# Optimization experiments

Hardware: AMD Instinct MI355X
Metric: run time of the kernel (lower is better)

The kernel has to match this reference:

```python
import jax, jax.numpy as jnp
import numpy as np

B, N, D = 8, 512, 512          # batch, seq_len, n_units (== d_in for residual)
H = 8                          # n_heads
DH = D // H                    # head dim
POS_CLIP = 60
EPS = 1e-7


def setup_inputs() -> dict:
    key = jax.random.key(0)
    ks = jax.random.split(key, 16)
    s = 0.02
    inp = {
        "query": jax.random.normal(ks[0], (B, N, D), dtype=jnp.float32),
        "valid_len": jax.random.randint(ks[1], (B,), 256, N + 1, dtype=jnp.int32),
        "Wq": jax.random.normal(ks[2], (D, D), dtype=jnp.float32) * s,
        "bq": jnp.zeros((D,), jnp.float32),
        "Wk": jax.random.normal(ks[3], (D, D), dtype=jnp.float32) * s,
        "bk": jnp.zeros((D,), jnp.float32),
        "Wv": jax.random.normal(ks[4], (D, D), dtype=jnp.float32) * s,
        "bv": jnp.zeros((D,), jnp.float32),
        "Wh": jax.random.normal(ks[5], (D, D), dtype=jnp.float32) * s,
        "bh": jnp.zeros((D,), jnp.float32),
        "pos_k": jax.random.uniform(ks[6], (2 * POS_CLIP + 1, DH), dtype=jnp.float32, minval=-0.05, maxval=0.05),
        "conv1_w": jax.random.normal(ks[7], (5, 5, H, 2 * H), dtype=jnp.float32) * s,  # HWIO
        "conv1_b": jnp.zeros((2 * H,), jnp.float32),
        "norm1_gamma": jnp.ones((2 * H,), jnp.float32),
        "norm1_beta": jnp.zeros((2 * H,), jnp.float32),
        "conv2_w": jax.random.normal(ks[8], (5, 5, 2 * H, H), dtype=jnp.float32) * s,
        "conv2_b": jnp.zeros((H,), jnp.float32),
        "ln_gamma": jnp.ones((D,), jnp.float32),
        "ln_beta": jnp.zeros((D,), jnp.float32),
    }
    return inp


def _conv_same(x, k, b):
    # x: [b, n, n, cin], k: [kh, kw, cin, cout] -> [b, n, n, cout]
    y = jax.lax.conv_general_dilated(x, k, window_strides=(1, 1), padding="SAME",
                                     dimension_numbers=("NHWC", "HWIO", "NHWC"))
    return y + b


def _norm_masked(x, valid_len, gamma, beta):
    # Norm(axes=[1,2]) with tf.nn.weighted_moments; mask over the query axis (axis 1).
    b, n, m, c = x.shape
    w = (jnp.arange(n)[None, :] < valid_len[:, None]).astype(x.dtype)  # [b, n]
    w4 = w[:, :, None, None]
    sw = valid_len.astype(x.dtype)[:, None, None, None] * m            # sum of broadcast weights
    mean = jnp.sum(w4 * x, axis=(1, 2), keepdims=True) / sw
    var = jnp.sum(w4 * (x - mean) ** 2, axis=(1, 2), keepdims=True) / sw
    return gamma * (x - mean) * jax.lax.rsqrt(var + EPS) + beta


def reference(query, valid_len, Wq, bq, Wk, bk, Wv, bv, Wh, bh, pos_k,
              conv1_w, conv1_b, norm1_gamma, norm1_beta, conv2_w, conv2_b,
              ln_gamma, ln_beta):
    b, n, d_in = query.shape
    # relative position indices (Shaw et al.), clipped to +/- POS_CLIP
    rel = jnp.clip(jnp.arange(n)[None, :] - jnp.arange(n)[:, None], -POS_CLIP, POS_CLIP) + POS_CLIP
    pos_enc = pos_k[rel]                                   # [n, n, dh]

    def heads(x):
        # tf.concat(tf.split(x, H, -1), 0): head-major blocks of size b
        return x.reshape(b, n, H, DH).transpose(2, 0, 1, 3)  # [h, b, n, dh]

    q = heads(query @ Wq + bq)
    k = heads(query @ Wk + bk)
    v = heads(query @ Wv + bv)

    scores = jnp.einsum("hbnd,hbmd->hbnm", q, k) + jnp.einsum("hbnd,nmd->hbnm", q, pos_enc)
    scores = scores / jnp.sqrt(jnp.asarray(DH, scores.dtype))

    # SelfCNN over attention maps: [b, n, n, h]
    maps = scores.transpose(1, 2, 3, 0)
    y = _conv_same(maps, conv1_w, conv1_b)
    y = _norm_masked(y, valid_len, norm1_gamma, norm1_beta)
    y = jax.nn.relu(y)
    y = _conv_same(y, conv2_w, conv2_b)                    # [b, n, n, h]
    scores = y.transpose(3, 0, 1, 2)                       # [h, b, n, m]

    seq_mask = jnp.arange(n)[None, :] < valid_len[:, None]  # [b, n] over key axis
    scores = jnp.where(seq_mask[None, :, None, :], scores, jnp.asarray(-1e12, scores.dtype))
    attn = jax.nn.softmax(scores, axis=-1)

    out = jnp.einsum("hbnm,hbmd->hbnd", attn, v)
    out = out.transpose(1, 2, 0, 3).reshape(b, n, H * DH)  # merge heads back
    out = out @ Wh + bh + query                            # residual

    mean = jnp.mean(out, axis=-1, keepdims=True)
    var = jnp.var(out, axis=-1, keepdims=True)
    return ln_gamma * (out - mean) * jax.lax.rsqrt(var + EPS) + ln_beta
```

## Files before the change

kernel.cpp:

```cpp
#include <hip/hip_runtime.h>

#define PC_ 60

typedef unsigned short u16;
typedef __attribute__((ext_vector_type(8))) short short8v;
typedef __attribute__((ext_vector_type(4))) float f32x4;

__device__ inline float bf2f(u16 u) {
    union { unsigned int i; float f; } x; x.i = ((unsigned)u) << 16; return x.f;
}
__device__ inline u16 f2bf(float f) {
    union { float f; unsigned int i; } x; x.f = f;
    unsigned int r = x.i + 0x7fff + ((x.i >> 16) & 1);
    return (u16)(r >> 16);
}
__device__ inline unsigned pk2(float a, float b) {
    return (unsigned)f2bf(a) | ((unsigned)f2bf(b) << 16);
}

__global__ __launch_bounds__(256) void k_prepx(const float* __restrict__ X, u16* __restrict__ Xb)
{
    const int i = (blockIdx.x * 256 + threadIdx.x) * 8;
    float4 a = *reinterpret_cast<const float4*>(X + i);
    float4 b = *reinterpret_cast<const float4*>(X + i + 4);
    *reinterpret_cast<uint4*>(Xb + i) =
        make_uint4(pk2(a.x, a.y), pk2(a.z, a.w), pk2(b.x, b.y), pk2(b.z, b.w));
}

__global__ __launch_bounds__(256) void k_prept(
    const float* __restrict__ W0, const float* __restrict__ W1,
    const float* __restrict__ W2, const float* __restrict__ W3,
    u16* __restrict__ T0, u16* __restrict__ T1, u16* __restrict__ T2, u16* __restrict__ T3)
{
    const int z = blockIdx.z;
    const float* W = (z == 0) ? W0 : (z == 1) ? W1 : (z == 2) ? W2 : W3;
    u16* T        = (z == 0) ? T0 : (z == 1) ? T1 : (z == 2) ? T2 : T3;
    __shared__ float ls[64 * 65];
    const int k0 = blockIdx.x * 64, n0 = blockIdx.y * 64;
    const int t = threadIdx.x;
#pragma unroll
    for (int i = 0; i < 16; ++i) {
        const int idx = t + i * 256, r = idx >> 6, c = idx & 63;
        ls[c * 65 + r] = W[(size_t)(k0 + r) * 512 + n0 + c];
    }
    __syncthreads();
#pragma unroll
    for (int i = 0; i < 16; ++i) {
        const int idx = t + i * 256, r = idx >> 6, c = idx & 63;
        T[(size_t)(n0 + r) * 512 + k0 + c] = f2bf(ls[r * 65 + c]);
    }
}

__global__ void k_wprep(const float* __restrict__ c1w, const float* __restrict__ c2w,
                        const float* __restrict__ pos_k,
                        u16* __restrict__ Wf1, u16* __restrict__ Wf2, u16* __restrict__ pos_kb)
{
    const int t = threadIdx.x;
    for (int s = t; s < 448; s += 256) {
        const int q = s >> 6, l = s & 63, lg = l >> 4, n = l & 15;
        const int G = q * 4 + lg;
        unsigned o[4];
#pragma unroll
        for (int u2 = 0; u2 < 4; ++u2) {
            float v0 = 0.f, v1 = 0.f;
            if (G < 25) {
                const int dn = G / 5, dm = G - dn * 5;
                v0 = c1w[((dn * 5 + dm) * 8 + u2 * 2 + 0) * 16 + n];
                v1 = c1w[((dn * 5 + dm) * 8 + u2 * 2 + 1) * 16 + n];
            }
            o[u2] = pk2(v0, v1);
        }
        *reinterpret_cast<uint4*>(&Wf1[s * 8]) = make_uint4(o[0], o[1], o[2], o[3]);
    }
    for (int s = t; s < 832; s += 256) {
        const int q = s >> 6, l = s & 63, lg = l >> 4, n = l & 15;
        const int G = q * 4 + lg;
        unsigned o[4];
#pragma unroll
        for (int u2 = 0; u2 < 4; ++u2) {
            float v0 = 0.f, v1 = 0.f;
            if (G < 50 && n < 8) {
                const int pos = G >> 1, h = G & 1;
                const int dn = pos / 5, dm = pos - dn * 5;
                v0 = c2w[((dn * 5 + dm) * 16 + h * 8 + u2 * 2 + 0) * 8 + n];
                v1 = c2w[((dn * 5 + dm) * 16 + h * 8 + u2 * 2 + 1) * 8 + n];
            }
            o[u2] = pk2(v0, v1);
        }
        *reinterpret_cast<uint4*>(&Wf2[s * 8]) = make_uint4(o[0], o[1], o[2], o[3]);
    }
    for (int s = t; s < 128 * 64; s += 256) {
        const int r = s >> 6;
        pos_kb[s] = (r < 121) ? f2bf(pos_k[s]) : (u16)0;
    }
}

__global__ __launch_bounds__(256) void k_qkvm(
    const u16* __restrict__ Xb,
    const u16* __restrict__ WT0, const u16* __restrict__ WT1, const u16* __restrict__ WT2,
    const float* __restrict__ b0, const float* __restrict__ b1, const float* __restrict__ b2,
    u16* __restrict__ Qb, u16* __restrict__ Kb, u16* __restrict__ Vt)
{
    const int z = blockIdx.z;
    const u16* WT    = (z == 0) ? WT0 : (z == 1) ? WT1 : WT2;
    const float* bias = (z == 0) ? b0 : (z == 1) ? b1 : b2;
    __shared__ __align__(16) u16 sh[18432];
    u16* As = sh; u16* Bs = sh + 9216;
    const int t = threadIdx.x, lane = t & 63, wave = t >> 6;
    const int wm = wave >> 1, wn = wave & 1;
    const int lg = lane >> 4, ln16 = lane & 15;
    const int m0 = blockIdx.x * 128, n0 = blockIdx.y * 128;
    f32x4 acc[4][4] = {};
    for (int k0 = 0; k0 < 512; k0 += 64) {
#pragma unroll
        for (int u = 0; u < 4; ++u) {
            const int chunk = u * 256 + t, row = chunk >> 3, ko = (chunk & 7) * 8;
            *reinterpret_cast<uint4*>(As + row * 72 + ko) =
                *reinterpret_cast<const uint4*>(Xb + (size_t)(m0 + row) * 512 + k0 + ko);
            *reinterpret_cast<uint4*>(Bs + row * 72 + ko) =
                *reinterpret_cast<const uint4*>(WT + (size_t)(n0 + row) * 512 + k0 + ko);
        }
        __syncthreads();
#pragma unroll
        for (int kk = 0; kk < 64; kk += 32) {
            short8v a[4], bfr[4];
#pragma unroll
            for (int mi = 0; mi < 4; ++mi)
                a[mi] = *reinterpret_cast<const short8v*>(As + (wm * 64 + mi * 16 + ln16) * 72 + kk + lg * 8);
#pragma unroll
            for (int ni = 0; ni < 4; ++ni)
                bfr[ni] = *reinterpret_cast<const short8v*>(Bs + (wn * 64 + ni * 16 + ln16) * 72 + kk + lg * 8);
#pragma unroll
            for (int mi = 0; mi < 4; ++mi)
#pragma unroll
                for (int ni = 0; ni < 4; ++ni)
                    acc[mi][ni] = __builtin_amdgcn_mfma_f32_16x16x32_bf16(a[mi], bfr[ni], acc[mi][ni], 0, 0, 0);
        }
        __syncthreads();
    }
    u16* Cs = sh + wave * 4608;
#pragma unroll
    for (int ni = 0; ni < 4; ++ni) {
        const float bv = bias[n0 + wn * 64 + ni * 16 + ln16];
#pragma unroll
        for (int mi = 0; mi < 4; ++mi)
#pragma unroll
            for (int r = 0; r < 4; ++r)
                Cs[(mi * 16 + lg * 4 + r) * 72 + ni * 16 + ln16] = f2bf(acc[mi][ni][r] + bv);
    }
    if (z < 2) {
        u16* O = (z == 0) ? Qb : Kb;
#pragma unroll
        for (int j = 0; j < 8; ++j) {
            const int chunk = j * 64 + lane, row = chunk >> 3, co = (chunk & 7) * 8;
            const int tok = m0 + wm * 64 + row;
            const int b = tok >> 9, n = tok & 511;
            const int cg = n0 + wn * 64 + co;
            const int h = cg >> 6, dh = cg & 63;
            *reinterpret_cast<uint4*>(O + ((size_t)((b * 8 + h) * 512 + n)) * 64 + dh) =
                *reinterpret_cast<const uint4*>(Cs + row * 72 + co);
        }
    } else {
#pragma unroll
        for (int j = 0; j < 8; ++j) {
            const int chunk = j * 64 + lane, dr = chunk >> 3, no8 = (chunk & 7) * 8;
            const int cg = n0 + wn * 64 + dr;
            const int h = cg >> 6, dh = cg & 63;
            const int tok = m0 + wm * 64 + no8;
            const int b = tok >> 9, n = tok & 511;
            u16 v[8];
#pragma unroll
            for (int e = 0; e < 8; ++e) v[e] = Cs[(no8 + e) * 72 + dr];
            uint4 o = make_uint4((unsigned)v[0] | ((unsigned)v[1] << 16),
                                 (unsigned)v[2] | ((unsigned)v[3] << 16),
                                 (unsigned)v[4] | ((unsigned)v[5] << 16),
                                 (unsigned)v[6] | ((unsigned)v[7] << 16));
            *reinterpret_cast<uint4*>(Vt + ((size_t)((b * 8 + h) * 64 + dh)) * 512 + n) = o;
        }
    }
}

__global__ __launch_bounds__(256) void k_qposm(
    const u16* __restrict__ Qb, const u16* __restrict__ pos_kb, u16* __restrict__ QP)
{
    __shared__ __align__(16) u16 sh[18432];
    u16* As = sh; u16* Bs = sh + 9216;
    const int t = threadIdx.x, lane = t & 63, wave = t >> 6;
    const int lg = lane >> 4, ln16 = lane & 15;
    const int n0 = blockIdx.x * 128, bh = blockIdx.y;
#pragma unroll
    for (int u = 0; u < 4; ++u) {
        const int chunk = u * 256 + t, row = chunk >> 3, ko = (chunk & 7) * 8;
        *reinterpret_cast<uint4*>(As + row * 72 + ko) =
            *reinterpret_cast<const uint4*>(Qb + ((size_t)(bh * 512 + n0 + row)) * 64 + ko);
        *reinterpret_cast<uint4*>(Bs + row * 72 + ko) =
            *reinterpret_cast<const uint4*>(pos_kb + (size_t)row * 64 + ko);
    }
    __syncthreads();
    f32x4 acc[2][8] = {};
#pragma unroll
    for (int kk = 0; kk < 64; kk += 32) {
        short8v a[2], bfr[8];
#pragma unroll
        for (int mi = 0; mi < 2; ++mi)
            a[mi] = *reinterpret_cast<const short8v*>(As + (wave * 32 + mi * 16 + ln16) * 72 + kk + lg * 8);
#pragma unroll
        for (int ni = 0; ni < 8; ++ni)
            bfr[ni] = *reinterpret_cast<const short8v*>(Bs + (ni * 16 + ln16) * 72 + kk + lg * 8);
#pragma unroll
        for (int mi = 0; mi < 2; ++mi)
#pragma unroll
            for (int ni = 0; ni < 8; ++ni)
                acc[mi][ni] = __builtin_amdgcn_mfma_f32_16x16x32_bf16(a[mi], bfr[ni], acc[mi][ni], 0, 0, 0);
    }
    __syncthreads();
    u16* Cs = sh + wave * 4352;
#pragma unroll
    for (int mi = 0; mi < 2; ++mi)
#pragma unroll
        for (int ni = 0; ni < 8; ++ni)
#pragma unroll
            for (int r = 0; r < 4; ++r)
                Cs[(mi * 16 + lg * 4 + r) * 136 + ni * 16 + ln16] = f2bf(acc[mi][ni][r]);
#pragma unroll
    for (int j = 0; j < 8; ++j) {
        const int chunk = j * 64 + lane, row = chunk >> 4, co = (chunk & 15) * 8;
        *reinterpret_cast<uint4*>(QP + ((size_t)(bh * 512 + n0 + wave * 32 + row)) * 128 + co) =
            *reinterpret_cast<const uint4*>(Cs + row * 136 + co);
    }
}

__global__ __launch_bounds__(256) void k_scoresm(
    const u16* __restrict__ Qb, const u16* __restrict__ Kb, const u16* __restrict__ QP,
    u16* __restrict__ S)
{
    __shared__ __align__(16) u16 sh[18432];
    u16* As = sh; u16* Bs = sh + 9216;
    const int t = threadIdx.x, lane = t & 63, wave = t >> 6;
    const int wm = wave >> 1, wn = wave & 1;
    const int lg = lane >> 4, ln16 = lane & 15;
    const int m0 = blockIdx.x * 128, n0 = blockIdx.y * 128, bh = blockIdx.z;
#pragma unroll
    for (int u = 0; u < 4; ++u) {
        const int chunk = u * 256 + t, row = chunk >> 3, ko = (chunk & 7) * 8;
        *reinterpret_cast<uint4*>(As + row * 72 + ko) =
            *reinterpret_cast<const uint4*>(Qb + ((size_t)(bh * 512 + n0 + row)) * 64 + ko);
        *reinterpret_cast<uint4*>(Bs + row * 72 + ko) =
            *reinterpret_cast<const uint4*>(Kb + ((size_t)(bh * 512 + m0 + row)) * 64 + ko);
    }
    __syncthreads();
    f32x4 acc[4][4] = {};
#pragma unroll
    for (int kk = 0; kk < 64; kk += 32) {
        short8v a[4], bfr[4];
#pragma unroll
        for (int mi = 0; mi < 4; ++mi)
            a[mi] = *reinterpret_cast<const short8v*>(As + (wm * 64 + mi * 16 + ln16) * 72 + kk + lg * 8);
#pragma unroll
        for (int ni = 0; ni < 4; ++ni)
            bfr[ni] = *reinterpret_cast<const short8v*>(Bs + (wn * 64 + ni * 16 + ln16) * 72 + kk + lg * 8);
#pragma unroll
        for (int mi = 0; mi < 4; ++mi)
#pragma unroll
            for (int ni = 0; ni < 4; ++ni)
                acc[mi][ni] = __builtin_amdgcn_mfma_f32_16x16x32_bf16(a[mi], bfr[ni], acc[mi][ni], 0, 0, 0);
    }
    __syncthreads();
    u16* QPs = sh;
#pragma unroll
    for (int u = 0; u < 8; ++u) {
        const int chunk = u * 256 + t, row = chunk >> 4, co = (chunk & 15) * 8;
        *reinterpret_cast<uint4*>(QPs + row * 128 + co) =
            *reinterpret_cast<const uint4*>(QP + ((size_t)(bh * 512 + n0 + row)) * 128 + co);
    }
    __syncthreads();
#pragma unroll
    for (int mi = 0; mi < 4; ++mi)
#pragma unroll
        for (int ni = 0; ni < 4; ++ni) {
            const int m_g = m0 + wn * 64 + ni * 16 + ln16;
#pragma unroll
            for (int r = 0; r < 4; ++r) {
                const int n_loc = wm * 64 + mi * 16 + lg * 4 + r;
                const int n_g = n0 + n_loc;
                int rel = m_g - n_g;
                rel = rel < -PC_ ? -PC_ : (rel > PC_ ? PC_ : rel);
                const float v = (acc[mi][ni][r] + bf2f(QPs[n_loc * 128 + rel + PC_])) * 0.125f;
                S[(size_t)bh * 262144 + (size_t)n_g * 512 + m_g] = f2bf(v);
            }
        }
}

__global__ __launch_bounds__(256) void k_conv1m(
    const u16* __restrict__ S, const u16* __restrict__ Wf,
    const float* __restrict__ bias, u16* __restrict__ Y,
    const int* __restrict__ VL, float* __restrict__ ST)
{
    __shared__ __align__(16) u16 xs[10368];
    __shared__ float wred[4][16][2];
    const int t = threadIdx.x;
    const int b = blockIdx.z;
    const int n0 = blockIdx.y * 32;
    const int m0 = blockIdx.x * 32;
    const u16* sp0 = S + (size_t)(b * 8) * 262144;
    for (int idx = t; idx < 1296; idx += 256) {
        const int r = idx / 36; const int c = idx - r * 36;
        const int gn = n0 - 2 + r, gm = m0 - 2 + c;
        uint4 pk = make_uint4(0, 0, 0, 0);
        if ((unsigned)gn < 512u && (unsigned)gm < 512u) {
            const u16* p = sp0 + (size_t)gn * 512 + gm;
            u16 v[8];
#pragma unroll
            for (int e = 0; e < 8; ++e) v[e] = p[(size_t)e * 262144];
            pk.x = (unsigned)v[0] | ((unsigned)v[1] << 16);
            pk.y = (unsigned)v[2] | ((unsigned)v[3] << 16);
            pk.z = (unsigned)v[4] | ((unsigned)v[5] << 16);
            pk.w = (unsigned)v[6] | ((unsigned)v[7] << 16);
        }
        *reinterpret_cast<uint4*>(&xs[idx * 8]) = pk;
    }
    const int lane = t & 63, wave = t >> 6;
    const int lg = lane >> 4, ln16 = lane & 15;
    short8v bq[7];
#pragma unroll
    for (int q = 0; q < 7; ++q)
        bq[q] = *reinterpret_cast<const short8v*>(&Wf[(q * 64 + lane) * 8]);
    int aoff[7];
#pragma unroll
    for (int q = 0; q < 7; ++q) {
        const int G = q * 4 + lg; const int p = (G < 25) ? G : 0;
        const int dn = p / 5, dm = p - dn * 5;
        aoff[q] = (dn * 36 + dm) * 8;
    }
    const float bs = bias[ln16];
    const int vl = VL[b];
    float sst = 0.f, sst2 = 0.f;
    __syncthreads();
    for (int i = 0; i < 16; ++i) {
        const int j = wave * 16 + i;
        const int tr = j >> 1, c0 = (j & 1) << 4;
        const int pb = (tr * 36 + c0 + ln16) * 8;
        f32x4 acc = {bs, bs, bs, bs};
#pragma unroll
        for (int q = 0; q < 7; ++q) {
            short8v a = *reinterpret_cast<const short8v*>(&xs[pb + aoff[q]]);
            acc = __builtin_amdgcn_mfma_f32_16x16x32_bf16(a, bq[q], acc, 0, 0, 0);
        }
        u16* yp = Y + (((size_t)(b * 512 + n0 + tr)) * 512 + (m0 + c0 + lg * 4)) * 16 + ln16;
        yp[0]  = f2bf(acc[0]); yp[16] = f2bf(acc[1]);
        yp[32] = f2bf(acc[2]); yp[48] = f2bf(acc[3]);
        if (n0 + tr < vl) {
            sst  += acc[0] + acc[1] + acc[2] + acc[3];
            sst2 += acc[0]*acc[0] + acc[1]*acc[1] + acc[2]*acc[2] + acc[3]*acc[3];
        }
    }
    sst  += __shfl_xor(sst, 16);  sst  += __shfl_xor(sst, 32);
    sst2 += __shfl_xor(sst2, 16); sst2 += __shfl_xor(sst2, 32);
    if (lane < 16) { wred[wave][lane][0] = sst; wred[wave][lane][1] = sst2; }
    __syncthreads();
    if (t < 16) {
        const float a  = wred[0][t][0] + wred[1][t][0] + wred[2][t][0] + wred[3][t][0];
        const float b2 = wred[0][t][1] + wred[1][t][1] + wred[2][t][1] + wred[3][t][1];
        atomicAdd(&ST[(b * 16 + t) * 2 + 0], a);
        atomicAdd(&ST[(b * 16 + t) * 2 + 1], b2);
    }
}

__global__ void k_statfin(const float* __restrict__ ST, const int* __restrict__ VL,
                          const float* __restrict__ g, const float* __restrict__ be,
                          float* __restrict__ ST2)
{
    const int i = threadIdx.x;
    if (i < 128) {
        const int b = i >> 4, c = i & 15;
        const float sw = (float)VL[b] * 512.f;
        const float mean = ST[i * 2] / sw;
        const float var = ST[i * 2 + 1] / sw - mean * mean;
        const float scale = g[c] * rsqrtf(var + 1e-7f);
        ST2[i * 2] = scale;
        ST2[i * 2 + 1] = be[c] - mean * scale;
    }
}

__global__ __launch_bounds__(256) void k_conv2m(
    const u16* __restrict__ Y, const float* __restrict__ ST2,
    const u16* __restrict__ Wf, const float* __restrict__ bias,
    u16* __restrict__ S2)
{
    __shared__ __align__(16) u16 xs[20736];
    const int t = threadIdx.x;
    const int b = blockIdx.z;
    const int n0 = blockIdx.y * 32, m0 = blockIdx.x * 32;
    float sc[16], shv[16];
#pragma unroll
    for (int ch = 0; ch < 16; ++ch) {
        sc[ch]  = ST2[(b * 16 + ch) * 2 + 0];
        shv[ch] = ST2[(b * 16 + ch) * 2 + 1];
    }
    for (int idx = t; idx < 1296; idx += 256) {
        const int r = idx / 36; const int c = idx - r * 36;
        const int gn = n0 - 2 + r, gm = m0 - 2 + c;
        uint4 p0 = make_uint4(0, 0, 0, 0), p1 = p0;
        if ((unsigned)gn < 512u && (unsigned)gm < 512u) {
            const u16* yp = Y + (((size_t)(b * 512 + gn)) * 512 + gm) * 16;
            const uint4 r0 = *reinterpret_cast<const uint4*>(yp);
            const uint4 r1 = *reinterpret_cast<const uint4*>(yp + 8);
            const unsigned w0[4] = {r0.x, r0.y, r0.z, r0.w};
            const unsigned w1[4] = {r1.x, r1.y, r1.z, r1.w};
            unsigned o0[4], o1[4];
#pragma unroll
            for (int u2 = 0; u2 < 4; ++u2) {
                const int ch = u2 * 2;
                float a0 = bf2f((u16)(w0[u2] & 0xffff));
                float a1 = bf2f((u16)(w0[u2] >> 16));
                a0 = fmaf(a0, sc[ch], shv[ch]);          a0 = a0 > 0.f ? a0 : 0.f;
                a1 = fmaf(a1, sc[ch + 1], shv[ch + 1]);  a1 = a1 > 0.f ? a1 : 0.f;
                o0[u2] = pk2(a0, a1);
                const int ch2 = 8 + u2 * 2;
                float b0 = bf2f((u16)(w1[u2] & 0xffff));
                float b1 = bf2f((u16)(w1[u2] >> 16));
                b0 = fmaf(b0, sc[ch2], shv[ch2]);          b0 = b0 > 0.f ? b0 : 0.f;
                b1 = fmaf(b1, sc[ch2 + 1], shv[ch2 + 1]);  b1 = b1 > 0.f ? b1 : 0.f;
                o1[u2] = pk2(b0, b1);
            }
            p0 = make_uint4(o0[0], o0[1], o0[2], o0[3]);
            p1 = make_uint4(o1[0], o1[1], o1[2], o1[3]);
        }
        *reinterpret_cast<uint4*>(&xs[idx * 8]) = p0;
        *reinterpret_cast<uint4*>(&xs[10368 + idx * 8]) = p1;
    }
    const int lane = t & 63, wave = t >> 6;
    const int lg = lane >> 4, ln16 = lane & 15;
    short8v bq[13];
#pragma unroll
    for (int q = 0; q < 13; ++q)
        bq[q] = *reinterpret_cast<const short8v*>(&Wf[(q * 64 + lane) * 8]);
    int aoff[13];
#pragma unroll
    for (int q = 0; q < 13; ++q) {
        const int G = q * 4 + lg; const int p = (G < 50) ? G : 0;
        const int pos = p >> 1, h = p & 1;
        const int dn = pos / 5, dm = pos - dn * 5;
        aoff[q] = h * 10368 + (dn * 36 + dm) * 8;
    }
    const float bs = (ln16 < 8) ? bias[ln16] : 0.f;
    __syncthreads();
    for (int i = 0; i < 16; ++i) {
        const int j = wave * 16 + i;
        const int tr = j >> 1, c0 = (j & 1) << 4;
        const int pb = (tr * 36 + c0 + ln16) * 8;
        f32x4 acc = {bs, bs, bs, bs};
#pragma unroll
        for (int q = 0; q < 13; ++q) {
            short8v a = *reinterpret_cast<const short8v*>(&xs[pb + aoff[q]]);
            acc = __builtin_amdgcn_mfma_f32_16x16x32_bf16(a, bq[q], acc, 0, 0, 0);
        }
        if (ln16 < 8) {
            uint2 o = make_uint2(pk2(acc[0], acc[1]), pk2(acc[2], acc[3]));
            *reinterpret_cast<uint2*>(
                &S2[(((size_t)(b * 8 + ln16)) * 512 + n0 + tr) * 512 + m0 + c0 + lg * 4]) = o;
        }
    }
}

__global__ __launch_bounds__(256) void k_softmax(u16* __restrict__ S,
                                                 const int* __restrict__ VL)
{
    const int row = blockIdx.x * 4 + (threadIdx.x >> 6);
    const int lane = threadIdx.x & 63;
    const int b = row >> 12;
    const int vl = VL[b];
    u16* p = S + (size_t)row * 512;
    uint4 v = *reinterpret_cast<const uint4*>(p + lane * 8);
    const unsigned w[4] = {v.x, v.y, v.z, v.w};
    float vals[8];
#pragma unroll
    for (int j = 0; j < 4; ++j) {
        vals[2 * j]     = bf2f((u16)(w[j] & 0xffff));
        vals[2 * j + 1] = bf2f((u16)(w[j] >> 16));
    }
    const int mbase = lane * 8;
    float mx = -3.0e38f;
#pragma unroll
    for (int j = 0; j < 8; ++j) {
        if (mbase + j >= vl) vals[j] = -3.0e38f;
        mx = fmaxf(mx, vals[j]);
    }
#pragma unroll
    for (int o = 32; o; o >>= 1) mx = fmaxf(mx, __shfl_xor(mx, o));
    float sum = 0.f;
#pragma unroll
    for (int j = 0; j < 8; ++j) {
        const float e = __expf(vals[j] - mx);
        vals[j] = e;
        sum += e;
    }
#pragma unroll
    for (int o = 32; o; o >>= 1) sum += __shfl_xor(sum, o);
    const float inv = 1.0f / sum;
    uint4 ov = make_uint4(pk2(vals[0] * inv, vals[1] * inv), pk2(vals[2] * inv, vals[3] * inv),
                          pk2(vals[4] * inv, vals[5] * inv), pk2(vals[6] * inv, vals[7] * inv));
    *reinterpret_cast<uint4*>(p + lane * 8) = ov;
}

__global__ __launch_bounds__(256) void k_avm(
    const u16* __restrict__ P, const u16* __restrict__ Vt, u16* __restrict__ X2)
{
    __shared__ __align__(16) u16 sh[13824];
    u16* As = sh; u16* Bs = sh + 9216;
    const int t = threadIdx.x, lane = t & 63, wave = t >> 6;
    const int lg = lane >> 4, ln16 = lane & 15;
    const int n0 = blockIdx.x * 128, bh = blockIdx.y;
    const int b = bh >> 3, h = bh & 7;
    f32x4 acc[2][4] = {};
    for (int k0 = 0; k0 < 512; k0 += 64) {
#pragma unroll
        for (int u = 0; u < 4; ++u) {
            const int chunk = u * 256 + t, row = chunk >> 3, ko = (chunk & 7) * 8;
            *reinterpret_cast<uint4*>(As + row * 72 + ko) =
                *reinterpret_cast<const uint4*>(P + ((size_t)(bh * 512 + n0 + row)) * 512 + k0 + ko);
        }
#pragma unroll
        for (int u = 0; u < 2; ++u) {
            const int chunk = u * 256 + t, row = chunk >> 3, ko = (chunk & 7) * 8;
            *reinterpret_cast<uint4*>(Bs + row * 72 + ko) =
                *reinterpret_cast<const uint4*>(Vt + ((size_t)(bh * 64 + row)) * 512 + k0 + ko);
        }
        __syncthreads();
#pragma unroll
        for (int kk = 0; kk < 64; kk += 32) {
            short8v a[2], bfr[4];
#pragma unroll
            for (int mi = 0; mi < 2; ++mi)
                a[mi] = *reinterpret_cast<const short8v*>(As + (wave * 32 + mi * 16 + ln16) * 72 + kk + lg * 8);
#pragma unroll
            for (int ni = 0; ni < 4; ++ni)
                bfr[ni] = *reinterpret_cast<const short8v*>(Bs + (ni * 16 + ln16) * 72 + kk + lg * 8);
#pragma unroll
            for (int mi = 0; mi < 2; ++mi)
#pragma unroll
                for (int ni = 0; ni < 4; ++ni)
                    acc[mi][ni] = __builtin_amdgcn_mfma_f32_16x16x32_bf16(a[mi], bfr[ni], acc[mi][ni], 0, 0, 0);
        }
        __syncthreads();
    }
    u16* Cs = sh + wave * 2304;
#pragma unroll
    for (int mi = 0; mi < 2; ++mi)
#pragma unroll
        for (int ni = 0; ni < 4; ++ni)
#pragma unroll
            for (int r = 0; r < 4; ++r)
                Cs[(mi * 16 + lg * 4 + r) * 72 + ni * 16 + ln16] = f2bf(acc[mi][ni][r]);
#pragma unroll
    for (int j = 0; j < 4; ++j) {
        const int chunk = j * 64 + lane, row = chunk >> 3, co = (chunk & 7) * 8;
        const int tn = n0 + wave * 32 + row;
        *reinterpret_cast<uint4*>(X2 + ((size_t)(b * 512 + tn)) * 512 + h * 64 + co) =
            *reinterpret_cast<const uint4*>(Cs + row * 72 + co);
    }
}

__global__ __launch_bounds__(256) void k_outm(
    const u16* __restrict__ X2, const u16* __restrict__ WT, const float* __restrict__ bias,
    const float* __restrict__ Xq, float* __restrict__ Pout)
{
    __shared__ __align__(16) u16 sh[18432];
    u16* As = sh; u16* Bs = sh + 9216;
    const int t = threadIdx.x, lane = t & 63, wave = t >> 6;
    const int wm = wave >> 1, wn = wave & 1;
    const int lg = lane >> 4, ln16 = lane & 15;
    const int m0 = blockIdx.x * 128, n0 = blockIdx.y * 128;
    f32x4 acc[4][4] = {};
    for (int k0 = 0; k0 < 512; k0 += 64) {
#pragma unroll
        for (int u = 0; u < 4; ++u) {
            const int chunk = u * 256 + t, row = chunk >> 3, ko = (chunk & 7) * 8;
            *reinterpret_cast<uint4*>(As + row * 72 + ko) =
                *reinterpret_cast<const uint4*>(X2 + (size_t)(m0 + row) * 512 + k0 + ko);
            *reinterpret_cast<uint4*>(Bs + row * 72 + ko) =
                *reinterpret_cast<const uint4*>(WT + (size_t)(n0 + row) * 512 + k0 + ko);
        }
        __syncthreads();
#pragma unroll
        for (int kk = 0; kk < 64; kk += 32) {
            short8v a[4], bfr[4];
#pragma unroll
            for (int mi = 0; mi < 4; ++mi)
                a[mi] = *reinterpret_cast<const short8v*>(As + (wm * 64 + mi * 16 + ln16) * 72 + kk + lg * 8);
#pragma unroll
            for (int ni = 0; ni < 4; ++ni)
                bfr[ni] = *reinterpret_cast<const short8v*>(Bs + (wn * 64 + ni * 16 + ln16) * 72 + kk + lg * 8);
#pragma unroll
            for (int mi = 0; mi < 4; ++mi)
#pragma unroll
                for (int ni = 0; ni < 4; ++ni)
                    acc[mi][ni] = __builtin_amdgcn_mfma_f32_16x16x32_bf16(a[mi], bfr[ni], acc[mi][ni], 0, 0, 0);
        }
        __syncthreads();
    }
#pragma unroll
    for (int ni = 0; ni < 4; ++ni) {
        const int cg = n0 + wn * 64 + ni * 16 + ln16;
        const float bv = bias[cg];
#pragma unroll
        for (int mi = 0; mi < 4; ++mi)
#pragma unroll
            for (int r = 0; r < 4; ++r) {
                const int tok = m0 + wm * 64 + mi * 16 + lg * 4 + r;
                Pout[(size_t)tok * 512 + cg] = acc[mi][ni][r] + bv + Xq[(size_t)tok * 512 + cg];
            }
    }
}

__global__ __launch_bounds__(256) void k_ln(
    const float* __restrict__ P, const float* __restrict__ g,
    const float* __restrict__ be, float* __restrict__ out)
{
    const int row = blockIdx.x * 4 + (threadIdx.x >> 6);
    const int lane = threadIdx.x & 63;
    const float* p = P + (size_t)row * 512;
    float4 v0 = reinterpret_cast<const float4*>(p)[lane];
    float4 v1 = reinterpret_cast<const float4*>(p)[64 + lane];
    float s = v0.x + v0.y + v0.z + v0.w + v1.x + v1.y + v1.z + v1.w;
#pragma unroll
    for (int o = 32; o; o >>= 1) s += __shfl_xor(s, o);
    const float mean = s * (1.0f / 512.0f);
    float d[8] = {v0.x - mean, v0.y - mean, v0.z - mean, v0.w - mean,
                  v1.x - mean, v1.y - mean, v1.z - mean, v1.w - mean};
    float s2 = 0.f;
#pragma unroll
    for (int j = 0; j < 8; ++j) s2 += d[j] * d[j];
#pragma unroll
    for (int o = 32; o; o >>= 1) s2 += __shfl_xor(s2, o);
    const float rstd = rsqrtf(s2 * (1.0f / 512.0f) + 1e-7f);
    float4 g0 = reinterpret_cast<const float4*>(g)[lane];
    float4 g1 = reinterpret_cast<const float4*>(g)[64 + lane];
    float4 b0 = reinterpret_cast<const float4*>(be)[lane];
    float4 b1 = reinterpret_cast<const float4*>(be)[64 + lane];
    float* op = out + (size_t)row * 512;
    reinterpret_cast<float4*>(op)[lane] =
        make_float4(d[0] * rstd * g0.x + b0.x, d[1] * rstd * g0.y + b0.y,
                    d[2] * rstd * g0.z + b0.z, d[3] * rstd * g0.w + b0.w);
    reinterpret_cast<float4*>(op)[64 + lane] =
        make_float4(d[4] * rstd * g1.x + b1.x, d[5] * rstd * g1.y + b1.y,
                    d[6] * rstd * g1.z + b1.z, d[7] * rstd * g1.w + b1.w);
}

extern "C" void kernel_launch(void* const* d_in, const int* in_sizes, int n_in,
                              void* d_out, int out_size, void* d_ws, size_t ws_size,
                              hipStream_t stream)
{
    const float* query = (const float*)d_in[0];
    const int*   VL    = (const int*)d_in[1];
    const float* Wq = (const float*)d_in[2];  const float* bq = (const float*)d_in[3];
    const float* Wk = (const float*)d_in[4];  const float* bk = (const float*)d_in[5];
    const float* Wv = (const float*)d_in[6];  const float* bv = (const float*)d_in[7];
    const float* Wh = (const float*)d_in[8];  const float* bh = (const float*)d_in[9];
    const float* pos_k = (const float*)d_in[10];
    const float* c1w = (const float*)d_in[11]; const float* c1b = (const float*)d_in[12];
    const float* n1g = (const float*)d_in[13]; const float* n1b = (const float*)d_in[14];
    const float* c2w = (const float*)d_in[15]; const float* c2b = (const float*)d_in[16];
    const float* lng = (const float*)d_in[17]; const float* lnb = (const float*)d_in[18];

    float* ws = (float*)d_ws;
    const size_t M1 = (size_t)1 << 20;
    u16* S1  = (u16*)ws;
    u16* Y1  = (u16*)(ws + 8 * M1);
    u16* Xb  = (u16*)(ws + 24 * M1);
    u16* Qb  = (u16*)(ws + 25 * M1);
    u16* Kb  = (u16*)(ws + 26 * M1);
    u16* Vt  = (u16*)(ws + 27 * M1);
    u16* QPb = (u16*)(ws + 28 * M1);
    u16* WqT = (u16*)(ws + 30 * M1);
    u16* WkT = WqT + 262144;
    u16* WvT = WkT + 262144;
    u16* WhT = WvT + 262144;
    u16* pos_kb = (u16*)(ws + 30 * M1 + 524288);
    u16* Wf1 = pos_kb + 8192;
    u16* Wf2 = Wf1 + 3584;
    float* ST  = ws + 31 * M1;
    float* ST2 = ST + 256;
    u16* X2 = Xb;
    float* Pout = ws + 28 * M1;

    hipMemsetAsync(ST, 0, 256 * sizeof(float), stream);

    k_prepx<<<1024, 256, 0, stream>>>(query, Xb);
    k_prept<<<dim3(8, 8, 4), 256, 0, stream>>>(Wq, Wk, Wv, Wh, WqT, WkT, WvT, WhT);
    k_wprep<<<1, 256, 0, stream>>>(c1w, c2w, pos_k, Wf1, Wf2, pos_kb);
    k_qkvm<<<dim3(32, 4, 3), 256, 0, stream>>>(Xb, WqT, WkT, WvT, bq, bk, bv, Qb, Kb, Vt);
    k_qposm<<<dim3(4, 64), 256, 0, stream>>>(Qb, pos_kb, QPb);
    k_scoresm<<<dim3(4, 4, 64), 256, 0, stream>>>(Qb, Kb, QPb, S1);
    k_conv1m<<<dim3(16, 16, 8), 256, 0, stream>>>(S1, Wf1, c1b, Y1, VL, ST);
    k_statfin<<<1, 128, 0, stream>>>(ST, VL, n1g, n1b, ST2);
    k_conv2m<<<dim3(16, 16, 8), 256, 0, stream>>>(Y1, ST2, Wf2, c2b, S1);
    k_softmax<<<8192, 256, 0, stream>>>(S1, VL);
    k_avm<<<dim3(4, 64), 256, 0, stream>>>(S1, Vt, X2);
    k_outm<<<dim3(32, 4), 256, 0, stream>>>(X2, WhT, bh, query, Pout);
    k_ln<<<1024, 256, 0, stream>>>(Pout, lng, lnb, (float*)d_out);
}
```

Measured before the change: 286.5 us.

## Fuse conv1 recompute into conv2, fuse softmax into AV, merge weight prep

Conv1 now runs twice. The first pass only gathers normalization statistics, writes no Y1, and skips tiles past valid_len. The second pass recomputes conv1 on a halo tile inside the conv2 kernel, so the 16-channel intermediate never goes to or from global memory. Softmax is folded into the AV GEMM: row max and sum are computed first and the probabilities are rebuilt on the fly while loading the A tiles. The weight-prep kernel is merged into the transpose kernel as an extra z-slice. This trades extra conv1 MFMA work, 67KB of dynamic shared memory (which limits occupancy) and a second exp pass for much less memory traffic and fewer launches.

```diff
diff --git a/kernel.cpp b/kernel.cpp
--- a/kernel.cpp
+++ b/kernel.cpp
@@ -30,14 +30,58 @@
 __global__ __launch_bounds__(256) void k_prept(
     const float* __restrict__ W0, const float* __restrict__ W1,
     const float* __restrict__ W2, const float* __restrict__ W3,
-    u16* __restrict__ T0, u16* __restrict__ T1, u16* __restrict__ T2, u16* __restrict__ T3)
+    u16* __restrict__ T0, u16* __restrict__ T1, u16* __restrict__ T2, u16* __restrict__ T3,
+    const float* __restrict__ c1w, const float* __restrict__ c2w,
+    const float* __restrict__ pos_k,
+    u16* __restrict__ Wf1, u16* __restrict__ Wf2, u16* __restrict__ pos_kb)
 {
     const int z = blockIdx.z;
+    const int t = threadIdx.x;
+    if (z == 4) {
+        if (blockIdx.x != 0 || blockIdx.y != 0) return;
+        for (int s = t; s < 448; s += 256) {
+            const int q = s >> 6, l = s & 63, lg = l >> 4, n = l & 15;
+            const int G = q * 4 + lg;
+            unsigned o[4];
+#pragma unroll
+            for (int u2 = 0; u2 < 4; ++u2) {
+                float v0 = 0.f, v1 = 0.f;
+                if (G < 25) {
+                    const int dn = G / 5, dm = G - dn * 5;
+                    v0 = c1w[((dn * 5 + dm) * 8 + u2 * 2 + 0) * 16 + n];
+                    v1 = c1w[((dn * 5 + dm) * 8 + u2 * 2 + 1) * 16 + n];
+                }
+                o[u2] = pk2(v0, v1);
+            }
+            *reinterpret_cast<uint4*>(&Wf1[s * 8]) = make_uint4(o[0], o[1], o[2], o[3]);
+        }
+        for (int s = t; s < 832; s += 256) {
+            const int q = s >> 6, l = s & 63, lg = l >> 4, n = l & 15;
+            const int G = q * 4 + lg;
+            unsigned o[4];
+#pragma unroll
+            for (int u2 = 0; u2 < 4; ++u2) {
+                float v0 = 0.f, v1 = 0.f;
+                if (G < 50 && n < 8) {
+                    const int pos = G >> 1, h = G & 1;
+                    const int dn = pos / 5, dm = pos - dn * 5;
+                    v0 = c2w[((dn * 5 + dm) * 16 + h * 8 + u2 * 2 + 0) * 8 + n];
+                    v1 = c2w[((dn * 5 + dm) * 16 + h * 8 + u2 * 2 + 1) * 8 + n];
+                }
+                o[u2] = pk2(v0, v1);
+            }
+            *reinterpret_cast<uint4*>(&Wf2[s * 8]) = make_uint4(o[0], o[1], o[2], o[3]);
+        }
+        for (int s = t; s < 128 * 64; s += 256) {
+            const int r = s >> 6;
+            pos_kb[s] = (r < 121) ? f2bf(pos_k[s]) : (u16)0;
+        }
+        return;
+    }
     const float* W = (z == 0) ? W0 : (z == 1) ? W1 : (z == 2) ? W2 : W3;
     u16* T        = (z == 0) ? T0 : (z == 1) ? T1 : (z == 2) ? T2 : T3;
     __shared__ float ls[64 * 65];
     const int k0 = blockIdx.x * 64, n0 = blockIdx.y * 64;
-    const int t = threadIdx.x;
 #pragma unroll
     for (int i = 0; i < 16; ++i) {
         const int idx = t + i * 256, r = idx >> 6, c = idx & 63;
@@ -48,50 +92,6 @@
     for (int i = 0; i < 16; ++i) {
         const int idx = t + i * 256, r = idx >> 6, c = idx & 63;
         T[(size_t)(n0 + r) * 512 + k0 + c] = f2bf(ls[r * 65 + c]);
-    }
-}
-
-__global__ void k_wprep(const float* __restrict__ c1w, const float* __restrict__ c2w,
-                        const float* __restrict__ pos_k,
-                        u16* __restrict__ Wf1, u16* __restrict__ Wf2, u16* __restrict__ pos_kb)
-{
-    const int t = threadIdx.x;
-    for (int s = t; s < 448; s += 256) {
-        const int q = s >> 6, l = s & 63, lg = l >> 4, n = l & 15;
-        const int G = q * 4 + lg;
-        unsigned o[4];
-#pragma unroll
-        for (int u2 = 0; u2 < 4; ++u2) {
-            float v0 = 0.f, v1 = 0.f;
-            if (G < 25) {
-                const int dn = G / 5, dm = G - dn * 5;
-                v0 = c1w[((dn * 5 + dm) * 8 + u2 * 2 + 0) * 16 + n];
-                v1 = c1w[((dn * 5 + dm) * 8 + u2 * 2 + 1) * 16 + n];
-            }
-            o[u2] = pk2(v0, v1);
-        }
-        *reinterpret_cast<uint4*>(&Wf1[s * 8]) = make_uint4(o[0], o[1], o[2], o[3]);
-    }
-    for (int s = t; s < 832; s += 256) {
-        const int q = s >> 6, l = s & 63, lg = l >> 4, n = l & 15;
-        const int G = q * 4 + lg;
-        unsigned o[4];
-#pragma unroll
-        for (int u2 = 0; u2 < 4; ++u2) {
-            float v0 = 0.f, v1 = 0.f;
-            if (G < 50 && n < 8) {
-                const int pos = G >> 1, h = G & 1;
-                const int dn = pos / 5, dm = pos - dn * 5;
-                v0 = c2w[((dn * 5 + dm) * 16 + h * 8 + u2 * 2 + 0) * 8 + n];
-                v1 = c2w[((dn * 5 + dm) * 16 + h * 8 + u2 * 2 + 1) * 8 + n];
-            }
-            o[u2] = pk2(v0, v1);
-        }
-        *reinterpret_cast<uint4*>(&Wf2[s * 8]) = make_uint4(o[0], o[1], o[2], o[3]);
-    }
-    for (int s = t; s < 128 * 64; s += 256) {
-        const int r = s >> 6;
-        pos_kb[s] = (r < 121) ? f2bf(pos_k[s]) : (u16)0;
     }
 }
 
@@ -291,10 +291,10 @@
         }
 }
 
-__global__ __launch_bounds__(256) void k_conv1m(
+__global__ __launch_bounds__(256) void k_stats1(
     const u16* __restrict__ S, const u16* __restrict__ Wf,
-    const float* __restrict__ bias, u16* __restrict__ Y,
-    const int* __restrict__ VL, float* __restrict__ ST)
+    const float* __restrict__ bias, const int* __restrict__ VL,
+    float* __restrict__ ST)
 {
     __shared__ __align__(16) u16 xs[10368];
     __shared__ float wred[4][16][2];
@@ -302,6 +302,8 @@
     const int b = blockIdx.z;
     const int n0 = blockIdx.y * 32;
     const int m0 = blockIdx.x * 32;
+    const int vl = VL[b];
+    if (n0 >= vl) return;
     const u16* sp0 = S + (size_t)(b * 8) * 262144;
     for (int idx = t; idx < 1296; idx += 256) {
         const int r = idx / 36; const int c = idx - r * 36;
@@ -333,7 +335,6 @@
         aoff[q] = (dn * 36 + dm) * 8;
     }
     const float bs = bias[ln16];
-    const int vl = VL[b];
     float sst = 0.f, sst2 = 0.f;
     __syncthreads();
     for (int i = 0; i < 16; ++i) {
@@ -346,9 +347,6 @@
             short8v a = *reinterpret_cast<const short8v*>(&xs[pb + aoff[q]]);
             acc = __builtin_amdgcn_mfma_f32_16x16x32_bf16(a, bq[q], acc, 0, 0, 0);
         }
-        u16* yp = Y + (((size_t)(b * 512 + n0 + tr)) * 512 + (m0 + c0 + lg * 4)) * 16 + ln16;
-        yp[0]  = f2bf(acc[0]); yp[16] = f2bf(acc[1]);
-        yp[32] = f2bf(acc[2]); yp[48] = f2bf(acc[3]);
         if (n0 + tr < vl) {
             sst  += acc[0] + acc[1] + acc[2] + acc[3];
             sst2 += acc[0]*acc[0] + acc[1]*acc[1] + acc[2]*acc[2] + acc[3]*acc[3];
@@ -382,78 +380,102 @@
     }
 }
 
-__global__ __launch_bounds__(256) void k_conv2m(
-    const u16* __restrict__ Y, const float* __restrict__ ST2,
-    const u16* __restrict__ Wf, const float* __restrict__ bias,
+__global__ __launch_bounds__(256) void k_fused12(
+    const u16* __restrict__ S, const float* __restrict__ ST2,
+    const u16* __restrict__ Wf1, const float* __restrict__ c1b,
+    const u16* __restrict__ Wf2, const float* __restrict__ c2b,
     u16* __restrict__ S2)
 {
-    __shared__ __align__(16) u16 xs[20736];
+    extern __shared__ __align__(16) u16 dsm[];
+    u16* xs = dsm;
+    u16* ys = dsm + 12800;
     const int t = threadIdx.x;
     const int b = blockIdx.z;
     const int n0 = blockIdx.y * 32, m0 = blockIdx.x * 32;
-    float sc[16], shv[16];
-#pragma unroll
-    for (int ch = 0; ch < 16; ++ch) {
-        sc[ch]  = ST2[(b * 16 + ch) * 2 + 0];
-        shv[ch] = ST2[(b * 16 + ch) * 2 + 1];
-    }
-    for (int idx = t; idx < 1296; idx += 256) {
-        const int r = idx / 36; const int c = idx - r * 36;
-        const int gn = n0 - 2 + r, gm = m0 - 2 + c;
-        uint4 p0 = make_uint4(0, 0, 0, 0), p1 = p0;
+    const u16* sp0 = S + (size_t)(b * 8) * 262144;
+    for (int idx = t; idx < 1600; idx += 256) {
+        const int r = idx / 40; const int c = idx - r * 40;
+        const int gn = n0 - 4 + r, gm = m0 - 4 + c;
+        uint4 pk = make_uint4(0, 0, 0, 0);
         if ((unsigned)gn < 512u && (unsigned)gm < 512u) {
-            const u16* yp = Y + (((size_t)(b * 512 + gn)) * 512 + gm) * 16;
-            const uint4 r0 = *reinterpret_cast<const uint4*>(yp);
-            const uint4 r1 = *reinterpret_cast<const uint4*>(yp + 8);
-            const unsigned w0[4] = {r0.x, r0.y, r0.z, r0.w};
-            const unsigned w1[4] = {r1.x, r1.y, r1.z, r1.w};
-            unsigned o0[4], o1[4];
-#pragma unroll
-            for (int u2 = 0; u2 < 4; ++u2) {
-                const int ch = u2 * 2;
-                float a0 = bf2f((u16)(w0[u2] & 0xffff));
-                float a1 = bf2f((u16)(w0[u2] >> 16));
-                a0 = fmaf(a0, sc[ch], shv[ch]);          a0 = a0 > 0.f ? a0 : 0.f;
-                a1 = fmaf(a1, sc[ch + 1], shv[ch + 1]);  a1 = a1 > 0.f ? a1 : 0.f;
-                o0[u2] = pk2(a0, a1);
-                const int ch2 = 8 + u2 * 2;
-                float b0 = bf2f((u16)(w1[u2] & 0xffff));
-                float b1 = bf2f((u16)(w1[u2] >> 16));
-                b0 = fmaf(b0, sc[ch2], shv[ch2]);          b0 = b0 > 0.f ? b0 : 0.f;
-                b1 = fmaf(b1, sc[ch2 + 1], shv[ch2 + 1]);  b1 = b1 > 0.f ? b1 : 0.f;
-                o1[u2] = pk2(b0, b1);
-            }
-            p0 = make_uint4(o0[0], o0[1], o0[2], o0[3]);
-            p1 = make_uint4(o1[0], o1[1], o1[2], o1[3]);
-        }
-        *reinterpret_cast<uint4*>(&xs[idx * 8]) = p0;
-        *reinterpret_cast<uint4*>(&xs[10368 + idx * 8]) = p1;
+            const u16* p = sp0 + (size_t)gn * 512 + gm;
+            u16 v[8];
+#pragma unroll
+            for (int e = 0; e < 8; ++e) v[e] = p[(size_t)e * 262144];
+            pk.x = (unsigned)v[0] | ((unsigned)v[1] << 16);
+            pk.y = (unsigned)v[2] | ((unsigned)v[3] << 16);
+            pk.z = (unsigned)v[4] | ((unsigned)v[5] << 16);
+            pk.w = (unsigned)v[6] | ((unsigned)v[7] << 16);
+        }
+        *reinterpret_cast<uint4*>(&xs[idx * 8]) = pk;
     }
     const int lane = t & 63, wave = t >> 6;
     const int lg = lane >> 4, ln16 = lane & 15;
-    short8v bq[13];
+    short8v bq1[7];
+#pragma unroll
+    for (int q = 0; q < 7; ++q)
+        bq1[q] = *reinterpret_cast<const short8v*>(&Wf1[(q * 64 + lane) * 8]);
+    int aoff1[7];
+#pragma unroll
+    for (int q = 0; q < 7; ++q) {
+        const int G = q * 4 + lg; const int p = (G < 25) ? G : 0;
+        const int dn = p / 5, dm = p - dn * 5;
+        aoff1[q] = (dn * 40 + dm) * 8;
+    }
+    const float bs1 = c1b[ln16];
+    const float scn = ST2[(b * 16 + ln16) * 2 + 0];
+    const float shn = ST2[(b * 16 + ln16) * 2 + 1];
+    const int yhalf = (ln16 >> 3) * 10368;
+    const int ych = ln16 & 7;
+    __syncthreads();
+    for (int i = 0; i < 21; ++i) {
+        const int j = i * 4 + wave;
+        if (j >= 81) break;
+        const int pa = j * 16 + ln16;
+        const int arow = pa / 36, acol = pa - arow * 36;
+        const int abase = (arow * 40 + acol) * 8;
+        f32x4 acc = {bs1, bs1, bs1, bs1};
+#pragma unroll
+        for (int q = 0; q < 7; ++q) {
+            short8v a = *reinterpret_cast<const short8v*>(&xs[abase + aoff1[q]]);
+            acc = __builtin_amdgcn_mfma_f32_16x16x32_bf16(a, bq1[q], acc, 0, 0, 0);
+        }
+#pragma unroll
+        for (int r = 0; r < 4; ++r) {
+            const int pr = j * 16 + lg * 4 + r;
+            const int prow = pr / 36, pcol = pr - prow * 36;
+            const int gn = n0 - 2 + prow, gm = m0 - 2 + pcol;
+            float v = 0.f;
+            if ((unsigned)gn < 512u && (unsigned)gm < 512u) {
+                v = fmaf(acc[r], scn, shn);
+                v = v > 0.f ? v : 0.f;
+            }
+            ys[pr * 8 + ych + yhalf] = f2bf(v);
+        }
+    }
+    short8v bq2[13];
 #pragma unroll
     for (int q = 0; q < 13; ++q)
-        bq[q] = *reinterpret_cast<const short8v*>(&Wf[(q * 64 + lane) * 8]);
-    int aoff[13];
+        bq2[q] = *reinterpret_cast<const short8v*>(&Wf2[(q * 64 + lane) * 8]);
+    int aoff2[13];
 #pragma unroll
     for (int q = 0; q < 13; ++q) {
         const int G = q * 4 + lg; const int p = (G < 50) ? G : 0;
         const int pos = p >> 1, h = p & 1;
         const int dn = pos / 5, dm = pos - dn * 5;
-        aoff[q] = h * 10368 + (dn * 36 + dm) * 8;
-    }
-    const float bs = (ln16 < 8) ? bias[ln16] : 0.f;
+        aoff2[q] = h * 10368 + (dn * 36 + dm) * 8;
+    }
+    const float bs2 = (ln16 < 8) ? c2b[ln16] : 0.f;
     __syncthreads();
     for (int i = 0; i < 16; ++i) {
         const int j = wave * 16 + i;
         const int tr = j >> 1, c0 = (j & 1) << 4;
         const int pb = (tr * 36 + c0 + ln16) * 8;
-        f32x4 acc = {bs, bs, bs, bs};
+        f32x4 acc = {bs2, bs2, bs2, bs2};
 #pragma unroll
         for (int q = 0; q < 13; ++q) {
-            short8v a = *reinterpret_cast<const short8v*>(&xs[pb + aoff[q]]);
-            acc = __builtin_amdgcn_mfma_f32_16x16x32_bf16(a, bq[q], acc, 0, 0, 0);
+            short8v a = *reinterpret_cast<const short8v*>(&ys[pb + aoff2[q]]);
+            acc = __builtin_amdgcn_mfma_f32_16x16x32_bf16(a, bq2[q], acc, 0, 0, 0);
         }
         if (ln16 < 8) {
             uint2 o = make_uint2(pk2(acc[0], acc[1]), pk2(acc[2], acc[3]));
@@ -463,62 +485,63 @@
     }
 }
 
-__global__ __launch_bounds__(256) void k_softmax(u16* __restrict__ S,
-                                                 const int* __restrict__ VL)
-{
-    const int row = blockIdx.x * 4 + (threadIdx.x >> 6);
-    const int lane = threadIdx.x & 63;
-    const int b = row >> 12;
-    const int vl = VL[b];
-    u16* p = S + (size_t)row * 512;
-    uint4 v = *reinterpret_cast<const uint4*>(p + lane * 8);
-    const unsigned w[4] = {v.x, v.y, v.z, v.w};
-    float vals[8];
-#pragma unroll
-    for (int j = 0; j < 4; ++j) {
-        vals[2 * j]     = bf2f((u16)(w[j] & 0xffff));
-        vals[2 * j + 1] = bf2f((u16)(w[j] >> 16));
-    }
-    const int mbase = lane * 8;
-    float mx = -3.0e38f;
-#pragma unroll
-    for (int j = 0; j < 8; ++j) {
-        if (mbase + j >= vl) vals[j] = -3.0e38f;
-        mx = fmaxf(mx, vals[j]);
-    }
-#pragma unroll
-    for (int o = 32; o; o >>= 1) mx = fmaxf(mx, __shfl_xor(mx, o));
-    float sum = 0.f;
-#pragma unroll
-    for (int j = 0; j < 8; ++j) {
-        const float e = __expf(vals[j] - mx);
-        vals[j] = e;
-        sum += e;
-    }
-#pragma unroll
-    for (int o = 32; o; o >>= 1) sum += __shfl_xor(sum, o);
-    const float inv = 1.0f / sum;
-    uint4 ov = make_uint4(pk2(vals[0] * inv, vals[1] * inv), pk2(vals[2] * inv, vals[3] * inv),
-                          pk2(vals[4] * inv, vals[5] * inv), pk2(vals[6] * inv, vals[7] * inv));
-    *reinterpret_cast<uint4*>(p + lane * 8) = ov;
-}
-
-__global__ __launch_bounds__(256) void k_avm(
-    const u16* __restrict__ P, const u16* __restrict__ Vt, u16* __restrict__ X2)
-{
-    __shared__ __align__(16) u16 sh[13824];
-    u16* As = sh; u16* Bs = sh + 9216;
+__global__ __launch_bounds__(256) void k_softav(
+    const u16* __restrict__ SL, const u16* __restrict__ Vt,
+    const int* __restrict__ VL, u16* __restrict__ X2)
+{
+    __shared__ __align__(16) u16 As[9216];
+    __shared__ __align__(16) u16 Bs[4608];
+    __shared__ float smx[128], siv[128];
     const int t = threadIdx.x, lane = t & 63, wave = t >> 6;
     const int lg = lane >> 4, ln16 = lane & 15;
     const int n0 = blockIdx.x * 128, bh = blockIdx.y;
     const int b = bh >> 3, h = bh & 7;
+    const int vl = VL[b];
+    const u16* Sp = SL + (size_t)bh * 262144;
+    for (int rr = 0; rr < 32; ++rr) {
+        const int row = wave * 32 + rr;
+        uint4 v = *reinterpret_cast<const uint4*>(Sp + (size_t)(n0 + row) * 512 + lane * 8);
+        const unsigned w[4] = {v.x, v.y, v.z, v.w};
+        float x[8];
+#pragma unroll
+        for (int j = 0; j < 4; ++j) {
+            x[2 * j]     = bf2f((u16)(w[j] & 0xffff));
+            x[2 * j + 1] = bf2f((u16)(w[j] >> 16));
+        }
+        const int mb = lane * 8;
+        float mx = -3.0e38f;
+#pragma unroll
+        for (int j = 0; j < 8; ++j) {
+            if (mb + j >= vl) x[j] = -3.0e38f;
+            mx = fmaxf(mx, x[j]);
+        }
+#pragma unroll
+        for (int o = 32; o; o >>= 1) mx = fmaxf(mx, __shfl_xor(mx, o));
+        float sm = 0.f;
+#pragma unroll
+        for (int j = 0; j < 8; ++j) sm += __expf(x[j] - mx);
+#pragma unroll
+        for (int o = 32; o; o >>= 1) sm += __shfl_xor(sm, o);
+        if (lane == 0) { smx[row] = mx; siv[row] = 1.0f / sm; }
+    }
+    __syncthreads();
     f32x4 acc[2][4] = {};
     for (int k0 = 0; k0 < 512; k0 += 64) {
 #pragma unroll
         for (int u = 0; u < 4; ++u) {
             const int chunk = u * 256 + t, row = chunk >> 3, ko = (chunk & 7) * 8;
-            *reinterpret_cast<uint4*>(As + row * 72 + ko) =
-                *reinterpret_cast<const uint4*>(P + ((size_t)(bh * 512 + n0 + row)) * 512 + k0 + ko);
+            uint4 raw = *reinterpret_cast<const uint4*>(Sp + (size_t)(n0 + row) * 512 + k0 + ko);
+            const unsigned w[4] = {raw.x, raw.y, raw.z, raw.w};
+            const float mxr = smx[row], ivr = siv[row];
+            unsigned o[4];
+#pragma unroll
+            for (int jj = 0; jj < 4; ++jj) {
+                const int m0i = k0 + ko + 2 * jj;
+                float a0 = (m0i     < vl) ? __expf(bf2f((u16)(w[jj] & 0xffff)) - mxr) * ivr : 0.f;
+                float a1 = (m0i + 1 < vl) ? __expf(bf2f((u16)(w[jj] >> 16))   - mxr) * ivr : 0.f;
+                o[jj] = pk2(a0, a1);
+            }
+            *reinterpret_cast<uint4*>(As + row * 72 + ko) = make_uint4(o[0], o[1], o[2], o[3]);
         }
 #pragma unroll
         for (int u = 0; u < 2; ++u) {
@@ -544,7 +567,7 @@
         }
         __syncthreads();
     }
-    u16* Cs = sh + wave * 2304;
+    u16* Cs = As + wave * 2304;
 #pragma unroll
     for (int mi = 0; mi < 2; ++mi)
 #pragma unroll
@@ -666,37 +689,36 @@
     float* ws = (float*)d_ws;
     const size_t M1 = (size_t)1 << 20;
     u16* S1  = (u16*)ws;
-    u16* Y1  = (u16*)(ws + 8 * M1);
-    u16* Xb  = (u16*)(ws + 24 * M1);
-    u16* Qb  = (u16*)(ws + 25 * M1);
-    u16* Kb  = (u16*)(ws + 26 * M1);
-    u16* Vt  = (u16*)(ws + 27 * M1);
-    u16* QPb = (u16*)(ws + 28 * M1);
-    u16* WqT = (u16*)(ws + 30 * M1);
+    u16* S2  = (u16*)(ws + 8 * M1);
+    u16* Xb  = (u16*)(ws + 16 * M1);
+    u16* Qb  = (u16*)(ws + 17 * M1);
+    u16* Kb  = (u16*)(ws + 18 * M1);
+    u16* Vt  = (u16*)(ws + 19 * M1);
+    u16* QPb = (u16*)(ws + 20 * M1);
+    u16* WqT = (u16*)(ws + 22 * M1);
     u16* WkT = WqT + 262144;
     u16* WvT = WkT + 262144;
     u16* WhT = WvT + 262144;
-    u16* pos_kb = (u16*)(ws + 30 * M1 + 524288);
+    u16* pos_kb = (u16*)(ws + 22 * M1 + 524288);
     u16* Wf1 = pos_kb + 8192;
     u16* Wf2 = Wf1 + 3584;
-    float* ST  = ws + 31 * M1;
+    float* ST  = ws + 23 * M1;
     float* ST2 = ST + 256;
     u16* X2 = Xb;
-    float* Pout = ws + 28 * M1;
+    float* Pout = ws + 20 * M1;
 
     hipMemsetAsync(ST, 0, 256 * sizeof(float), stream);
 
     k_prepx<<<1024, 256, 0, stream>>>(query, Xb);
-    k_prept<<<dim3(8, 8, 4), 256, 0, stream>>>(Wq, Wk, Wv, Wh, WqT, WkT, WvT, WhT);
-    k_wprep<<<1, 256, 0, stream>>>(c1w, c2w, pos_k, Wf1, Wf2, pos_kb);
+    k_prept<<<dim3(8, 8, 5), 256, 0, stream>>>(Wq, Wk, Wv, Wh, WqT, WkT, WvT, WhT,
+                                               c1w, c2w, pos_k, Wf1, Wf2, pos_kb);
     k_qkvm<<<dim3(32, 4, 3), 256, 0, stream>>>(Xb, WqT, WkT, WvT, bq, bk, bv, Qb, Kb, Vt);
     k_qposm<<<dim3(4, 64), 256, 0, stream>>>(Qb, pos_kb, QPb);
     k_scoresm<<<dim3(4, 4, 64), 256, 0, stream>>>(Qb, Kb, QPb, S1);
-    k_conv1m<<<dim3(16, 16, 8), 256, 0, stream>>>(S1, Wf1, c1b, Y1, VL, ST);
+    k_stats1<<<dim3(16, 16, 8), 256, 0, stream>>>(S1, Wf1, c1b, VL, ST);
     k_statfin<<<1, 128, 0, stream>>>(ST, VL, n1g, n1b, ST2);
-    k_conv2m<<<dim3(16, 16, 8), 256, 0, stream>>>(Y1, ST2, Wf2, c2b, S1);
-    k_softmax<<<8192, 256, 0, stream>>>(S1, VL);
-    k_avm<<<dim3(4, 64), 256, 0, stream>>>(S1, Vt, X2);
+    k_fused12<<<dim3(16, 16, 8), 256, 67072, stream>>>(S1, ST2, Wf1, c1b, Wf2, c2b, S2);
+    k_softav<<<dim3(4, 64), 256, 0, stream>>>(S2, Vt, VL, X2);
     k_outm<<<dim3(32, 4), 256, 0, stream>>>(X2, WhT, bh, query, Pout);
     k_ln<<<1024, 256, 0, stream>>>(Pout, lng, lnb, (float*)d_out);
 }
```

Measured after the change: 326.1 us. 13.8% more time.
